# Optimization experiments

Hardware: AMD Instinct MI355X
Metric: run time of the kernel (lower is better)

Reference implementation:

```python
import jax, jax.numpy as jnp
import numpy as np

KS = 3
ST = 1


def _windows(x, ks, st):
    """im2col sliding windows: (bs, c, h, w) -> (bs, c, H', W', ks, ks)
    where windows[b,c,i,j,k,f] = x[b,c, i*st+k, j*st+f] (matches torch as_strided)."""
    bs, c, h, w = x.shape
    Hp = (h - ks) // st + 1
    Wp = (w - ks) // st + 1
    return jnp.stack(
        [jnp.stack([x[:, :, k:k + Hp * st:st, f:f + Wp * st:st] for f in range(ks)], axis=-1)
         for k in range(ks)], axis=-2)


def setup_inputs() -> dict:
    key = jax.random.key(0)
    k1, k2, k3 = jax.random.split(key, 3)
    x = jax.random.normal(k1, (16, 16, 64, 512), dtype=jnp.float32)
    points = jax.random.normal(k2, (16, 3, 64, 512), dtype=jnp.float32)
    kernel = jax.random.normal(k3, (32, 16, 4), dtype=jnp.float32) * 0.05
    return {"x": x, "kernel": kernel, "points": points}


def reference(x, kernel, points):
    ks, st = KS, ST
    # (bs, in_c, H', W', ks, ks) overlapping patches of features and xyz coords
    strided_x = _windows(x, ks, st)
    strided_pts = _windows(points, ks, st)
    bd = ks // 2 if st == 1 else ks // 4
    # center point of each window: (bs, 3, H', W')
    ctr = points[:, :, bd:-bd, bd:-bd][:, :, ::st, ::st]
    # point-relative coordinates per window element: (bs, 3, H', W', ks, ks)
    rel_pts = ctr[..., None, None] - strided_pts
    # homogeneous coordinate -> d = 4
    rel_pts = jnp.concatenate([rel_pts, jnp.ones_like(rel_pts[:, :1])], axis=1)
    # kernel: (out_c, in_c, 4)
    return jnp.einsum('bdhwkf,bihwkf,oid->bohw', rel_pts, strided_x, kernel)
```

## Files before the change

kernel.cpp:

```cpp
#include <hip/hip_runtime.h>
#include <hip/hip_bf16.h>


#define HH 64
#define WW 512
#define HP 62
#define WP 510
#define IC 16
#define OC 32
#define BS 16
#define RB 4
#define TR (RB + 2)
#define TC 64
#define LC 68
#define NPL 19
#define CPR 17
#define NROWS (NPL * TR)
#define NCHUNK (NROWS * CPR)

typedef __attribute__((ext_vector_type(8))) short short8;
typedef __attribute__((ext_vector_type(4))) float f32x4;

static __device__ __forceinline__ short f2bf(float f) {
    union { __hip_bfloat16 h; short s; } u;
    u.h = __float2bfloat16(f);
    return u.s;
}

__global__ __launch_bounds__(256) void flex_conv_v9(
    const float* __restrict__ x, const float* __restrict__ kern,
    const float* __restrict__ pts, float* __restrict__ out)
{
    __shared__ float lds[NPL * TR * LC];

    const int tid = threadIdx.x;
    const int j0 = blockIdx.x * TC;
    int i0 = blockIdx.y * RB;
    if (i0 > HP - RB) i0 = HP - RB;
    const int b = blockIdx.z;

    const float* xb = x + (size_t)b * IC * HH * WW;
    const float* pb = pts + (size_t)b * 3 * HH * WW;

    #pragma unroll
    for (int rnd = 0; rnd < 8; ++rnd) {
        const int cid = tid + rnd * 256;
        if (cid < NCHUNK) {
            const int row = cid / CPR;
            const int chunk = cid - row * CPR;
            const int plane = row / TR;
            const int rr = row - plane * TR;
            const float* base = (plane < IC)
                ? (xb + (size_t)plane * HH * WW)
                : (pb + (size_t)(plane - IC) * HH * WW);
            int gcol = j0 + chunk * 4;
            if (gcol > WW - 4) gcol = WW - 4;
            const float* src = base + (size_t)(i0 + rr) * WW + gcol;
            __builtin_amdgcn_global_load_lds(
                (const __attribute__((address_space(1))) void*)src,
                (__attribute__((address_space(3))) void*)(&lds[row * LC + chunk * 4]),
                16, 0, 0);
        }
    }

    const int lane = tid & 63;
    const int wave = tid >> 6;
    const int p = lane & 15;
    const int c = lane >> 4;
    const int tc = wave * 16 + p;

    short8 a0lo, a0hi, a1lo, a1hi;
    {
        const float4* k0v = (const float4*)(kern + (size_t)p * 64 + c * 8);
        const float4* k1v = (const float4*)(kern + (size_t)(16 + p) * 64 + c * 8);
        float4 v0a = k0v[0], v0b = k0v[1], v0c = k0v[8], v0d = k0v[9];
        float4 v1a = k1v[0], v1b = k1v[1], v1c = k1v[8], v1d = k1v[9];
        a0lo[0]=f2bf(v0a.x); a0lo[1]=f2bf(v0a.y); a0lo[2]=f2bf(v0a.z); a0lo[3]=f2bf(v0a.w);
        a0lo[4]=f2bf(v0b.x); a0lo[5]=f2bf(v0b.y); a0lo[6]=f2bf(v0b.z); a0lo[7]=f2bf(v0b.w);
        a0hi[0]=f2bf(v0c.x); a0hi[1]=f2bf(v0c.y); a0hi[2]=f2bf(v0c.z); a0hi[3]=f2bf(v0c.w);
        a0hi[4]=f2bf(v0d.x); a0hi[5]=f2bf(v0d.y); a0hi[6]=f2bf(v0d.z); a0hi[7]=f2bf(v0d.w);
        a1lo[0]=f2bf(v1a.x); a1lo[1]=f2bf(v1a.y); a1lo[2]=f2bf(v1a.z); a1lo[3]=f2bf(v1a.w);
        a1lo[4]=f2bf(v1b.x); a1lo[5]=f2bf(v1b.y); a1lo[6]=f2bf(v1b.z); a1lo[7]=f2bf(v1b.w);
        a1hi[0]=f2bf(v1c.x); a1hi[1]=f2bf(v1c.y); a1hi[2]=f2bf(v1c.z); a1hi[3]=f2bf(v1c.w);
        a1hi[4]=f2bf(v1d.x); a1hi[5]=f2bf(v1d.y); a1hi[6]=f2bf(v1d.z); a1hi[7]=f2bf(v1d.w);
    }

    __syncthreads();

    float xs[4][RB], px0[4][RB], px1[4][RB], px2[4][RB];
    #pragma unroll
    for (int t = 0; t < 4; ++t)
        #pragma unroll
        for (int q = 0; q < RB; ++q) { xs[t][q]=0.f; px0[t][q]=0.f; px1[t][q]=0.f; px2[t][q]=0.f; }
    float c0[RB], c1[RB], c2[RB];

    #pragma unroll
    for (int rr = 0; rr < TR; ++rr) {
        const float* lp0 = &lds[(IC * TR + rr) * LC + tc];
        const float* lp1 = &lds[((IC + 1) * TR + rr) * LC + tc];
        const float* lp2 = &lds[((IC + 2) * TR + rr) * LC + tc];
        const float pa0 = lp0[0], pm0 = lp0[1], pz0 = lp0[2];
        const float pa1 = lp1[0], pm1 = lp1[1], pz1 = lp1[2];
        const float pa2 = lp2[0], pm2 = lp2[1], pz2 = lp2[2];
        if (rr >= 1 && rr <= RB) { c0[rr-1] = pm0; c1[rr-1] = pm1; c2[rr-1] = pm2; }
        #pragma unroll
        for (int t = 0; t < 4; ++t) {
            const int ic = (t >> 1) * 8 + 2 * c + (t & 1);
            const float* lx = &lds[(ic * TR + rr) * LC + tc];
            const float x0 = lx[0], x1 = lx[1], x2 = lx[2];
            const float rsx = x0 + x1 + x2;
            float r0 = pa0 * x0; r0 = fmaf(pm0, x1, r0); r0 = fmaf(pz0, x2, r0);
            float r1 = pa1 * x0; r1 = fmaf(pm1, x1, r1); r1 = fmaf(pz1, x2, r1);
            float r2 = pa2 * x0; r2 = fmaf(pm2, x1, r2); r2 = fmaf(pz2, x2, r2);
            #pragma unroll
            for (int q = 0; q < RB; ++q) {
                if (rr >= q && rr <= q + 2) {
                    xs[t][q] += rsx; px0[t][q] += r0; px1[t][q] += r1; px2[t][q] += r2;
                }
            }
        }
    }

    const int j = j0 + tc;
    #pragma unroll
    for (int q = 0; q < RB; ++q) {
        short8 blo, bhi;
        #pragma unroll
        for (int t = 0; t < 4; ++t) {
            const short t0 = f2bf(fmaf(c0[q], xs[t][q], -px0[t][q]));
            const short t1 = f2bf(fmaf(c1[q], xs[t][q], -px1[t][q]));
            const short t2 = f2bf(fmaf(c2[q], xs[t][q], -px2[t][q]));
            const short t3 = f2bf(xs[t][q]);
            const int s = (t & 1) * 4;
            if (t < 2) { blo[s+0]=t0; blo[s+1]=t1; blo[s+2]=t2; blo[s+3]=t3; }
            else       { bhi[s+0]=t0; bhi[s+1]=t1; bhi[s+2]=t2; bhi[s+3]=t3; }
        }
        f32x4 acc0 = {0.f,0.f,0.f,0.f}, acc1 = {0.f,0.f,0.f,0.f};
        acc0 = __builtin_amdgcn_mfma_f32_16x16x32_bf16(a0lo, blo, acc0, 0, 0, 0);
        acc0 = __builtin_amdgcn_mfma_f32_16x16x32_bf16(a0hi, bhi, acc0, 0, 0, 0);
        acc1 = __builtin_amdgcn_mfma_f32_16x16x32_bf16(a1lo, blo, acc1, 0, 0, 0);
        acc1 = __builtin_amdgcn_mfma_f32_16x16x32_bf16(a1hi, bhi, acc1, 0, 0, 0);
        if (j < WP) {
            float* ob = out + (size_t)b * OC * HP * WP + (size_t)(i0 + q) * WP + j;
            #pragma unroll
            for (int r = 0; r < 4; ++r) {
                const int o = c * 4 + r;
                ob[(size_t)o * HP * WP]        = acc0[r];
                ob[(size_t)(o + 16) * HP * WP] = acc1[r];
            }
        }
    }
}

extern "C" void kernel_launch(void* const* d_in, const int* in_sizes, int n_in,
                              void* d_out, int out_size, void* d_ws, size_t ws_size,
                              hipStream_t stream)
{
    const float* x    = (const float*)d_in[0];
    const float* kern = (const float*)d_in[1];
    const float* pts  = (const float*)d_in[2];
    float* out = (float*)d_out;

    dim3 block(256, 1, 1);
    dim3 grid(WW / TC, (HP + RB - 1) / RB, BS);
    flex_conv_v9<<<grid, block, 0, stream>>>(x, kern, pts, out);
}
```

Before: 110.4 us.

## Give each wave a private LDS tile and replace block barrier with per-wave waitcnt

```diff
diff --git a/kernel.cpp b/kernel.cpp
--- a/kernel.cpp
+++ b/kernel.cpp
@@ -12,11 +12,12 @@
 #define RB 4
 #define TR (RB + 2)
 #define TC 64
-#define LC 68
 #define NPL 19
-#define CPR 17
-#define NROWS (NPL * TR)
-#define NCHUNK (NROWS * CPR)
+#define WPL 20
+#define WCH 5
+#define WROWS (NPL * TR)
+#define WCHUNK (WROWS * WCH)
+#define WSLOT (WROWS * WPL)
 
 typedef __attribute__((ext_vector_type(8))) short short8;
 typedef __attribute__((ext_vector_type(4))) float f32x4;
@@ -27,47 +28,48 @@
     return u.s;
 }
 
-__global__ __launch_bounds__(256) void flex_conv_v9(
+__global__ __launch_bounds__(256) void flex_conv_v10(
     const float* __restrict__ x, const float* __restrict__ kern,
     const float* __restrict__ pts, float* __restrict__ out)
 {
-    __shared__ float lds[NPL * TR * LC];
+    __shared__ float lds[4 * WSLOT];
 
     const int tid = threadIdx.x;
+    const int lane = tid & 63;
+    const int wave = tid >> 6;
+    const int p = lane & 15;
+    const int c = lane >> 4;
+
     const int j0 = blockIdx.x * TC;
     int i0 = blockIdx.y * RB;
     if (i0 > HP - RB) i0 = HP - RB;
     const int b = blockIdx.z;
+    const int wcb = j0 + wave * 16;
 
     const float* xb = x + (size_t)b * IC * HH * WW;
     const float* pb = pts + (size_t)b * 3 * HH * WW;
+    float* const wl = lds + wave * WSLOT;
 
     #pragma unroll
-    for (int rnd = 0; rnd < 8; ++rnd) {
-        const int cid = tid + rnd * 256;
-        if (cid < NCHUNK) {
-            const int row = cid / CPR;
-            const int chunk = cid - row * CPR;
+    for (int rnd = 0; rnd < 9; ++rnd) {
+        const int cid = lane + rnd * 64;
+        if (cid < WCHUNK) {
+            const int row = cid / WCH;
+            const int chunk = cid - row * WCH;
             const int plane = row / TR;
             const int rr = row - plane * TR;
             const float* base = (plane < IC)
                 ? (xb + (size_t)plane * HH * WW)
                 : (pb + (size_t)(plane - IC) * HH * WW);
-            int gcol = j0 + chunk * 4;
+            int gcol = wcb + chunk * 4;
             if (gcol > WW - 4) gcol = WW - 4;
             const float* src = base + (size_t)(i0 + rr) * WW + gcol;
             __builtin_amdgcn_global_load_lds(
                 (const __attribute__((address_space(1))) void*)src,
-                (__attribute__((address_space(3))) void*)(&lds[row * LC + chunk * 4]),
+                (__attribute__((address_space(3))) void*)(wl + cid * 4),
                 16, 0, 0);
         }
     }
-
-    const int lane = tid & 63;
-    const int wave = tid >> 6;
-    const int p = lane & 15;
-    const int c = lane >> 4;
-    const int tc = wave * 16 + p;
 
     short8 a0lo, a0hi, a1lo, a1hi;
     {
@@ -85,7 +87,8 @@
         a1hi[4]=f2bf(v1d.x); a1hi[5]=f2bf(v1d.y); a1hi[6]=f2bf(v1d.z); a1hi[7]=f2bf(v1d.w);
     }
 
-    __syncthreads();
+    asm volatile("s_waitcnt vmcnt(0)" ::: "memory");
+    __builtin_amdgcn_sched_barrier(0);
 
     float xs[4][RB], px0[4][RB], px1[4][RB], px2[4][RB];
     #pragma unroll
@@ -96,9 +99,9 @@
 
     #pragma unroll
     for (int rr = 0; rr < TR; ++rr) {
-        const float* lp0 = &lds[(IC * TR + rr) * LC + tc];
-        const float* lp1 = &lds[((IC + 1) * TR + rr) * LC + tc];
-        const float* lp2 = &lds[((IC + 2) * TR + rr) * LC + tc];
+        const float* lp0 = wl + ((IC + 0) * TR + rr) * WPL + p;
+        const float* lp1 = wl + ((IC + 1) * TR + rr) * WPL + p;
+        const float* lp2 = wl + ((IC + 2) * TR + rr) * WPL + p;
         const float pa0 = lp0[0], pm0 = lp0[1], pz0 = lp0[2];
         const float pa1 = lp1[0], pm1 = lp1[1], pz1 = lp1[2];
         const float pa2 = lp2[0], pm2 = lp2[1], pz2 = lp2[2];
@@ -106,7 +109,7 @@
         #pragma unroll
         for (int t = 0; t < 4; ++t) {
             const int ic = (t >> 1) * 8 + 2 * c + (t & 1);
-            const float* lx = &lds[(ic * TR + rr) * LC + tc];
+            const float* lx = wl + (ic * TR + rr) * WPL + p;
             const float x0 = lx[0], x1 = lx[1], x2 = lx[2];
             const float rsx = x0 + x1 + x2;
             float r0 = pa0 * x0; r0 = fmaf(pm0, x1, r0); r0 = fmaf(pz0, x2, r0);
@@ -121,7 +124,7 @@
         }
     }
 
-    const int j = j0 + tc;
+    const int j = wcb + p;
     #pragma unroll
     for (int q = 0; q < RB; ++q) {
         short8 blo, bhi;
@@ -163,5 +166,5 @@
 
     dim3 block(256, 1, 1);
     dim3 grid(WW / TC, (HP + RB - 1) / RB, BS);
-    flex_conv_v9<<<grid, block, 0, stream>>>(x, kern, pts, out);
+    flex_conv_v10<<<grid, block, 0, stream>>>(x, kern, pts, out);
 }
```

Result: slower. 115.3 us (+4.5%).
